# Kernel optimization log

Measured on AMD Instinct MI355X. Metric: run time of the kernel, lower is better.

## Reference

```python
import jax, jax.numpy as jnp
import numpy as np

# Static config (matches init_kwargs / spatial layout)
SHAPES = ((64, 64), (32, 32), (16, 16))   # (H, W) per level, bev=256 at /4,/8,/16
B, HEADS, LEVELS, POINTS, C = 2, 8, 3, 4, 256
HD = C // HEADS
NV = sum(h * w for h, w in SHAPES)        # 5376
NQ = NV
TP = HEADS * LEVELS * POINTS              # 96


def setup_inputs() -> dict:
    key = jax.random.key(0)
    ks = jax.random.split(key, 10)
    s = 1.0 / np.sqrt(C)
    inp = {
        'query': jax.random.normal(ks[0], (B, NQ, C), dtype=jnp.float32),
        'reference_points': jax.random.uniform(ks[1], (B, NQ, 2), dtype=jnp.float32),
        'value': jax.random.normal(ks[2], (B, NV, C), dtype=jnp.float32),
        'Wv': jax.random.normal(ks[3], (C, C), dtype=jnp.float32) * s,
        'bv': jnp.zeros((C,), dtype=jnp.float32),
        # offset proj: small scale so sampling stays local-ish (orig init is 0)
        'Woff': jax.random.normal(ks[4], (TP * 2, C), dtype=jnp.float32) * (0.02 * s),
        'boff': jnp.zeros((TP * 2,), dtype=jnp.float32),
        'Wa': jax.random.normal(ks[5], (TP, C), dtype=jnp.float32) * s,
        'ba': jnp.zeros((TP,), dtype=jnp.float32),
        'Wo': jax.random.normal(ks[6], (C, C), dtype=jnp.float32) * s,
        'bo': jnp.zeros((C,), dtype=jnp.float32),
    }
    return inp


def _msda(query, reference_points, value, Wv, bv, Woff, boff, Wa, ba, Wo, bo):
    Bb, nq, _ = query.shape
    # value projection -> per-head values
    v = (value @ Wv.T + bv).reshape(Bb, NV, HEADS, HD)
    # sampling offsets: (B, NQ, HEADS, LEVELS, POINTS, 2)
    off = (query @ Woff.T + boff).reshape(Bb, nq, HEADS, LEVELS, POINTS, 2)
    # attention weights: softmax over LEVELS*POINTS jointly
    a = (query @ Wa.T + ba).reshape(Bb, nq, HEADS, LEVELS * POINTS)
    a = jax.nn.softmax(a, axis=-1).reshape(Bb, nq, HEADS, LEVELS, POINTS)
    # sampling locations in [0,1] (clamp matches torch .clamp(0,1))
    loc = jnp.clip(reference_points[:, :, None, None, None, :] + off, 0.0, 1.0)

    out = jnp.zeros((Bb, HEADS, nq, HD), dtype=query.dtype)
    start = 0
    for lvl, (H, W) in enumerate(SHAPES):
        n = H * W
        # (B, HEADS, H*W, HD) flattened level feature map per head
        vl = jnp.transpose(v[:, start:start + n].reshape(Bb, H, W, HEADS, HD),
                           (0, 3, 1, 2, 4)).reshape(Bb, HEADS, n, HD)
        loc_l = loc[:, :, :, lvl]                     # (B, NQ, HEADS, K, 2)
        # align_corners=False unnormalization: ((g+1)*size - 1)/2 with g=2*loc-1
        x = loc_l[..., 0] * W - 0.5
        y = loc_l[..., 1] * H - 0.5
        x0 = jnp.floor(x)
        y0 = jnp.floor(y)
        wx1 = x - x0
        wy1 = y - y0
        x0i = x0.astype(jnp.int32)
        y0i = y0.astype(jnp.int32)
        acc = jnp.zeros((Bb, HEADS, nq * POINTS, HD), dtype=query.dtype)
        for dy in (0, 1):
            for dx in (0, 1):
                ix = x0i + dx
                iy = y0i + dy
                wgt = (wx1 if dx else 1.0 - wx1) * (wy1 if dy else 1.0 - wy1)
                # zero padding outside the map (padding_mode='zeros')
                valid = (ix >= 0) & (ix < W) & (iy >= 0) & (iy < H)
                idx = jnp.clip(iy, 0, H - 1) * W + jnp.clip(ix, 0, W - 1)
                idx_t = jnp.transpose(idx, (0, 2, 1, 3)).reshape(Bb, HEADS, nq * POINTS)
                g = jnp.take_along_axis(vl, idx_t[..., None], axis=2)  # (B,H,NQ*K,HD)
                w_t = jnp.transpose(wgt * valid.astype(wgt.dtype),
                                    (0, 2, 1, 3)).reshape(Bb, HEADS, nq * POINTS, 1)
                acc = acc + g * w_t
        aw = jnp.transpose(a[:, :, :, lvl], (0, 2, 1, 3)).reshape(Bb, HEADS, nq * POINTS, 1)
        out = out + (acc * aw).reshape(Bb, HEADS, nq, POINTS, HD).sum(axis=3)
        start += n
    out = jnp.transpose(out, (0, 2, 1, 3)).reshape(Bb, nq, C)
    return out @ Wo.T + bo


def reference(query, reference_points, value, Wv, bv, Woff, boff, Wa, ba, Wo, bo):
    return _msda(query, reference_points, value, Wv, bv, Woff, boff, Wa, ba, Wo, bo)
```

## Files before the change

kernel.cpp:

```cpp
#include <hip/hip_runtime.h>
#include <hip/hip_bf16.h>
#include <cmath>

#define BATCH   2
#define NQ      5376
#define NV      5376
#define CDIM    256
#define HEADS   8
#define HD      32
#define LEVELS  3
#define POINTS  4
#define TP      96
#define MROWS   (BATCH*NQ)
#define NOFF    (TP*2)
#define NQA     (NOFF+TP)

typedef __attribute__((ext_vector_type(8))) short bf16x8;
typedef __attribute__((ext_vector_type(4))) float f32x4;
typedef unsigned short u16;
typedef unsigned int   u32;

#define AS1 __attribute__((address_space(1)))
#define AS3 __attribute__((address_space(3)))

__device__ __forceinline__ void g2lds16(const void* g, void* l) {
    __builtin_amdgcn_global_load_lds((const AS1 void*)g, (AS3 void*)l, 16, 0, 0);
}

__device__ __forceinline__ u16 bf_of(float f) {
    union { __hip_bfloat16 h; u16 s; } u;
    u.h = __float2bfloat16(f);
    return u.s;
}
__device__ __forceinline__ float bf_back(u16 s) {
    return __uint_as_float((u32)s << 16);
}

__device__ __forceinline__ ushort4 cvt_hi(float4 v) {
    ushort4 h;
    h.x = bf_of(v.x); h.y = bf_of(v.y); h.z = bf_of(v.z); h.w = bf_of(v.w);
    return h;
}
__device__ __forceinline__ ushort4 cvt_lo(float4 v, ushort4 h) {
    ushort4 l;
    l.x = bf_of(v.x - bf_back(h.x));
    l.y = bf_of(v.y - bf_back(h.y));
    l.z = bf_of(v.z - bf_back(h.z));
    l.w = bf_of(v.w - bf_back(h.w));
    return l;
}

#define GBM 64
#define GBN 64
#define GBK 32


#define VBLOCKS (168 * 4)
__global__ __launch_bounds__(256) void gemm_vqa_kernel(
    const float* __restrict__ value, const float* __restrict__ Wv,
    const float* __restrict__ bv, u16* __restrict__ vOut,
    const float* __restrict__ query, const float* __restrict__ Woff,
    const float* __restrict__ Wa,
    const float* __restrict__ boff, const float* __restrict__ ba,
    u16* __restrict__ offOut, u16* __restrict__ aOut)
{
    __shared__ u16 sAh[GBM * GBK];
    __shared__ u16 sAl[GBM * GBK];
    __shared__ u16 sBh[GBN * GBK];

    const int bid = blockIdx.x;
    const bool vpath = bid < VBLOCKS;
    int m0, n0;
    if (vpath) { m0 = (bid >> 2) * GBM;           n0 = (bid & 3) * GBN; }
    else       { const int b2 = bid - VBLOCKS;
                 m0 = (b2 / 5) * GBM;             n0 = (b2 % 5) * GBN; }

    const int tid  = threadIdx.x;
    const int lane = tid & 63;
    const int wave = tid >> 6;
    const int wr   = wave & 1;
    const int wc   = wave >> 1;
    const int qm   = lane & 15;
    const int quad = lane >> 4;

    const int srow = tid >> 2;
    const int sc   = (tid & 3) * 8;

    const float* Asrc = (vpath ? value : query) + (size_t)(m0 + srow) * CDIM;
    const float* Bsrc;
    if (vpath) {
        Bsrc = Wv + (size_t)(n0 + srow) * CDIM;
    } else {
        const int rg = min(n0 + srow, NQA - 1);
        Bsrc = (rg < NOFF) ? (Woff + (size_t)rg * CDIM)
                           : (Wa + (size_t)(rg - NOFF) * CDIM);
    }

    f32x4 acc[2][2];
    #pragma unroll
    for (int i = 0; i < 2; ++i)
        #pragma unroll
        for (int j = 0; j < 2; ++j)
            acc[i][j] = (f32x4){0.f, 0.f, 0.f, 0.f};

    for (int k0 = 0; k0 < CDIM; k0 += GBK) {
        const float4 a0 = *reinterpret_cast<const float4*>(&Asrc[k0 + sc]);
        const float4 a1 = *reinterpret_cast<const float4*>(&Asrc[k0 + sc + 4]);
        const ushort4 ah0 = cvt_hi(a0), ah1 = cvt_hi(a1);
        *reinterpret_cast<ushort4*>(&sAh[srow * GBK + sc])     = ah0;
        *reinterpret_cast<ushort4*>(&sAh[srow * GBK + sc + 4]) = ah1;
        if (vpath) {
            *reinterpret_cast<ushort4*>(&sAl[srow * GBK + sc])     = cvt_lo(a0, ah0);
            *reinterpret_cast<ushort4*>(&sAl[srow * GBK + sc + 4]) = cvt_lo(a1, ah1);
        }
        const float4 b0 = *reinterpret_cast<const float4*>(&Bsrc[k0 + sc]);
        const float4 b1 = *reinterpret_cast<const float4*>(&Bsrc[k0 + sc + 4]);
        *reinterpret_cast<ushort4*>(&sBh[srow * GBK + sc])     = cvt_hi(b0);
        *reinterpret_cast<ushort4*>(&sBh[srow * GBK + sc + 4]) = cvt_hi(b1);
        __syncthreads();

        bf16x8 fah[2], fal[2], fbh[2];
        #pragma unroll
        for (int x = 0; x < 2; ++x) {
            const int rm = wr * 32 + x * 16 + qm;
            const int rn = wc * 32 + x * 16 + qm;
            fah[x] = *reinterpret_cast<const bf16x8*>(&sAh[rm * GBK + quad * 8]);
            fbh[x] = *reinterpret_cast<const bf16x8*>(&sBh[rn * GBK + quad * 8]);
            if (vpath)
                fal[x] = *reinterpret_cast<const bf16x8*>(&sAl[rm * GBK + quad * 8]);
        }
        #pragma unroll
        for (int mi = 0; mi < 2; ++mi)
            #pragma unroll
            for (int ni = 0; ni < 2; ++ni) {
                acc[mi][ni] = __builtin_amdgcn_mfma_f32_16x16x32_bf16(
                    fah[mi], fbh[ni], acc[mi][ni], 0, 0, 0);
                if (vpath)
                    acc[mi][ni] = __builtin_amdgcn_mfma_f32_16x16x32_bf16(
                        fal[mi], fbh[ni], acc[mi][ni], 0, 0, 0);
            }
        __syncthreads();
    }

    #pragma unroll
    for (int mi = 0; mi < 2; ++mi) {
        #pragma unroll
        for (int ni = 0; ni < 2; ++ni) {
            const int n = n0 + wc * 32 + ni * 16 + qm;
            if (vpath) {
                const float bn = bv[n];
                #pragma unroll
                for (int r = 0; r < 4; ++r) {
                    const int m = m0 + wr * 32 + mi * 16 + quad * 4 + r;
                    const float val = acc[mi][ni][r] + bn;
                    const int b = m / NV, rr = m - b * NV;
                    const int h = n >> 5, c = n & 31;
                    vOut[(((size_t)b * HEADS + h) * NV + rr) * HD + c] = bf_of(val);
                }
            } else {
                if (n >= NQA) continue;
                const float bn = (n < NOFF) ? boff[n] : ba[n - NOFF];
                #pragma unroll
                for (int r = 0; r < 4; ++r) {
                    const int m = m0 + wr * 32 + mi * 16 + quad * 4 + r;
                    const float val = acc[mi][ni][r] + bn;
                    if (n < NOFF)
                        offOut[(size_t)m * NOFF + n] = bf_of(val);
                    else
                        aOut[(size_t)m * TP + (n - NOFF)] = bf_of(val);
                }
            }
        }
    }
}

__global__ __launch_bounds__(256) void gemm_out_kernel(
    const u16* __restrict__ Ah, const u16* __restrict__ Al,
    const float* __restrict__ Wo, const float* __restrict__ bias,
    float* __restrict__ Cout)
{
    __shared__ u16 sAh[GBM * GBK];
    __shared__ u16 sAl[GBM * GBK];
    __shared__ u16 sBh[GBN * GBK];

    const int bid = blockIdx.x;
    const int m0 = (bid >> 2) * GBM;
    const int n0 = (bid & 3) * GBN;

    const int tid  = threadIdx.x;
    const int lane = tid & 63;
    const int wave = tid >> 6;
    const int wr   = wave & 1;
    const int wc   = wave >> 1;
    const int qm   = lane & 15;
    const int quad = lane >> 4;

    const int arow = (wave << 4) + (lane >> 2);
    const int ak   = (lane & 3) * 8;
    const int srow = tid >> 2;
    const int sc   = (tid & 3) * 8;
    const float* Bsrc = Wo + (size_t)(n0 + srow) * CDIM;

    f32x4 acc[2][2];
    #pragma unroll
    for (int i = 0; i < 2; ++i)
        #pragma unroll
        for (int j = 0; j < 2; ++j)
            acc[i][j] = (f32x4){0.f, 0.f, 0.f, 0.f};

    for (int k0 = 0; k0 < CDIM; k0 += GBK) {
        const size_t ga = (size_t)(m0 + arow) * CDIM + k0 + ak;
        g2lds16(Ah + ga, sAh + wave * 512);
        g2lds16(Al + ga, sAl + wave * 512);
        const float4 b0 = *reinterpret_cast<const float4*>(&Bsrc[k0 + sc]);
        const float4 b1 = *reinterpret_cast<const float4*>(&Bsrc[k0 + sc + 4]);
        *reinterpret_cast<ushort4*>(&sBh[srow * GBK + sc])     = cvt_hi(b0);
        *reinterpret_cast<ushort4*>(&sBh[srow * GBK + sc + 4]) = cvt_hi(b1);
        __syncthreads();

        bf16x8 fah[2], fal[2], fbh[2];
        #pragma unroll
        for (int x = 0; x < 2; ++x) {
            const int rm = wr * 32 + x * 16 + qm;
            const int rn = wc * 32 + x * 16 + qm;
            fah[x] = *reinterpret_cast<const bf16x8*>(&sAh[rm * GBK + quad * 8]);
            fal[x] = *reinterpret_cast<const bf16x8*>(&sAl[rm * GBK + quad * 8]);
            fbh[x] = *reinterpret_cast<const bf16x8*>(&sBh[rn * GBK + quad * 8]);
        }
        #pragma unroll
        for (int mi = 0; mi < 2; ++mi)
            #pragma unroll
            for (int ni = 0; ni < 2; ++ni) {
                acc[mi][ni] = __builtin_amdgcn_mfma_f32_16x16x32_bf16(
                    fah[mi], fbh[ni], acc[mi][ni], 0, 0, 0);
                acc[mi][ni] = __builtin_amdgcn_mfma_f32_16x16x32_bf16(
                    fal[mi], fbh[ni], acc[mi][ni], 0, 0, 0);
            }
        __syncthreads();
    }

    #pragma unroll
    for (int mi = 0; mi < 2; ++mi) {
        #pragma unroll
        for (int ni = 0; ni < 2; ++ni) {
            const int n = n0 + wc * 32 + ni * 16 + qm;
            const float bn = bias[n];
            #pragma unroll
            for (int r = 0; r < 4; ++r) {
                const int m = m0 + wr * 32 + mi * 16 + quad * 4 + r;
                Cout[(size_t)m * CDIM + n] = acc[mi][ni][r] + bn;
            }
        }
    }
}

__global__ __launch_bounds__(256) void msda_core_kernel(
    const u16* __restrict__ off,
    const u16* __restrict__ alog,
    const float* __restrict__ refp,
    const u16*   __restrict__ v,
    u16* __restrict__ t_hi,
    u16* __restrict__ t_lo)
{
    const int tid  = threadIdx.x;
    const int half = tid >> 7;
    const int ht   = tid & 127;
    const int bq   = blockIdx.x * 2 + half;
    const int b    = bq / NQ;

    __shared__ float s_w[2][TP];
    __shared__ int   s_idx[2][TP][4];
    __shared__ float s_twt[2][TP][4];

    if (ht < TP) s_w[half][ht] = bf_back(alog[(size_t)bq * TP + ht]);
    __syncthreads();

    if (ht < HEADS) {
        float mx = -1e30f;
        #pragma unroll
        for (int i = 0; i < 12; ++i) mx = fmaxf(mx, s_w[half][ht * 12 + i]);
        float e[12];
        float sum = 0.f;
        #pragma unroll
        for (int i = 0; i < 12; ++i) {
            e[i] = expf(s_w[half][ht * 12 + i] - mx);
            sum += e[i];
        }
        const float inv = 1.f / sum;
        #pragma unroll
        for (int i = 0; i < 12; ++i) s_w[half][ht * 12 + i] = e[i] * inv;
    }
    __syncthreads();

    if (ht < TP) {
        const int j  = ht;
        const int jj = j % 12;
        const int l  = jj >> 2;
        const int Wl    = (l == 0) ? 64 : (l == 1) ? 32 : 16;
        const int start = (l == 0) ? 0 : (l == 1) ? 4096 : 5120;

        const float refx = refp[(size_t)bq * 2 + 0];
        const float refy = refp[(size_t)bq * 2 + 1];
        const float ox = bf_back(off[(size_t)bq * NOFF + j * 2 + 0]);
        const float oy = bf_back(off[(size_t)bq * NOFF + j * 2 + 1]);
        const float lx = fminf(fmaxf(refx + ox, 0.f), 1.f) * (float)Wl - 0.5f;
        const float ly = fminf(fmaxf(refy + oy, 0.f), 1.f) * (float)Wl - 0.5f;
        const float fx0 = floorf(lx), fy0 = floorf(ly);
        const int   x0  = (int)fx0,   y0  = (int)fy0;
        const float wx1 = lx - fx0,   wy1 = ly - fy0;
        const float wx0 = 1.f - wx1,  wy0 = 1.f - wy1;
        const float aw  = s_w[half][j];

        #pragma unroll
        for (int k = 0; k < 4; ++k) {
            const int dx = k & 1, dy = k >> 1;
            const int xi = x0 + dx, yi = y0 + dy;
            const bool ok = (xi >= 0) & (xi < Wl) & (yi >= 0) & (yi < Wl);
            const int xc = min(max(xi, 0), Wl - 1);
            const int yc = min(max(yi, 0), Wl - 1);
            s_idx[half][j][k] = (start + yc * Wl + xc) * (HD * 2);
            const float wxy = (dx ? wx1 : wx0) * (dy ? wy1 : wy0);
            s_twt[half][j][k] = ok ? aw * wxy : 0.f;
        }
    }
    __syncthreads();

    const int h   = ht >> 4;
    const int sub = ht & 15;
    const int q   = sub & 7;
    const int rep = sub >> 3;
    const char* vb = (const char*)v + (((size_t)b * HEADS + h) * NV) * (HD * 2) + q * 8;

    float acc0 = 0.f, acc1 = 0.f, acc2 = 0.f, acc3 = 0.f;
    #pragma unroll
    for (int g = 0; g < 3; ++g) {
        uint2 raw[8];
        float wt[8];
        #pragma unroll
        for (int pp = 0; pp < 2; ++pp) {
            const int j = h * 12 + rep * 6 + g * 2 + pp;
            const int4   ix = *reinterpret_cast<const int4*>(&s_idx[half][j][0]);
            const float4 tw = *reinterpret_cast<const float4*>(&s_twt[half][j][0]);
            raw[pp * 4 + 0] = *reinterpret_cast<const uint2*>(vb + ix.x);
            raw[pp * 4 + 1] = *reinterpret_cast<const uint2*>(vb + ix.y);
            raw[pp * 4 + 2] = *reinterpret_cast<const uint2*>(vb + ix.z);
            raw[pp * 4 + 3] = *reinterpret_cast<const uint2*>(vb + ix.w);
            wt[pp * 4 + 0] = tw.x; wt[pp * 4 + 1] = tw.y;
            wt[pp * 4 + 2] = tw.z; wt[pp * 4 + 3] = tw.w;
        }
        #pragma unroll
        for (int k = 0; k < 8; ++k) {
            acc0 += wt[k] * __uint_as_float(raw[k].x << 16);
            acc1 += wt[k] * __uint_as_float(raw[k].x & 0xffff0000u);
            acc2 += wt[k] * __uint_as_float(raw[k].y << 16);
            acc3 += wt[k] * __uint_as_float(raw[k].y & 0xffff0000u);
        }
    }

    acc0 += __shfl_xor(acc0, 8);
    acc1 += __shfl_xor(acc1, 8);
    acc2 += __shfl_xor(acc2, 8);
    acc3 += __shfl_xor(acc3, 8);

    if (rep == 0) {
        ushort4 hh, ll;
        hh.x = bf_of(acc0); ll.x = bf_of(acc0 - bf_back(hh.x));
        hh.y = bf_of(acc1); ll.y = bf_of(acc1 - bf_back(hh.y));
        hh.z = bf_of(acc2); ll.z = bf_of(acc2 - bf_back(hh.z));
        hh.w = bf_of(acc3); ll.w = bf_of(acc3 - bf_back(hh.w));
        const size_t base = (size_t)bq * CDIM + h * HD + q * 4;
        *reinterpret_cast<ushort4*>(t_hi + base) = hh;
        *reinterpret_cast<ushort4*>(t_lo + base) = ll;
    }
}

extern "C" void kernel_launch(void* const* d_in, const int* in_sizes, int n_in,
                              void* d_out, int out_size, void* d_ws, size_t ws_size,
                              hipStream_t stream)
{
    const float* query = (const float*)d_in[0];
    const float* refp  = (const float*)d_in[1];
    const float* value = (const float*)d_in[2];
    const float* Wv    = (const float*)d_in[3];
    const float* bv    = (const float*)d_in[4];
    const float* Woff  = (const float*)d_in[5];
    const float* boff  = (const float*)d_in[6];
    const float* Wa    = (const float*)d_in[7];
    const float* ba    = (const float*)d_in[8];
    const float* Wo    = (const float*)d_in[9];
    const float* bo    = (const float*)d_in[10];
    float* out = (float*)d_out;

    char* w = (char*)d_ws;
    const size_t SZ_T = (size_t)MROWS * CDIM * 2;
    u16* v_bf16 = (u16*)(w);
    u16* t_hi   = (u16*)(w + 1 * SZ_T);
    u16* t_lo   = (u16*)(w + 2 * SZ_T);
    u16* ws_off = (u16*)(w + 3 * SZ_T);
    u16* ws_a   = (u16*)(w + 3 * SZ_T + (size_t)MROWS * NOFF * 2);

    const dim3 blk(256);

    gemm_vqa_kernel<<<dim3(VBLOCKS + (MROWS / GBM) * 5), blk, 0, stream>>>(
        value, Wv, bv, v_bf16,
        query, Woff, Wa, boff, ba, ws_off, ws_a);

    msda_core_kernel<<<dim3(MROWS / 2), blk, 0, stream>>>(
        ws_off, ws_a, refp, v_bf16, t_hi, t_lo);

    gemm_out_kernel<<<dim3((MROWS / GBM) * 4), blk, 0, stream>>>(
        t_hi, t_lo, Wo, bo, out);
}
```

Before: 138.9 us.

## Drop lo-part split for sampled output and widen gather to 16-byte loads

The low-residual bf16 tensor for the sampled attention output is removed, so the output GEMM does one MFMA per tile instead of two and reads half the activation data. The sampling kernel now handles four queries per block with 64 threads each, and each lane gathers 8 channels with 16-byte loads instead of 4 with 8-byte loads. This cuts memory traffic and instruction count in both the sampling and the output projection, at the cost of lower precision in the output GEMM inputs.

Result: faster. 135.6 us (-2.4%).

```diff
diff --git a/kernel.cpp b/kernel.cpp
--- a/kernel.cpp
+++ b/kernel.cpp
@@ -53,7 +53,6 @@
 #define GBM 64
 #define GBN 64
 #define GBK 32
-
 
 #define VBLOCKS (168 * 4)
 __global__ __launch_bounds__(256) void gemm_vqa_kernel(
@@ -175,12 +174,11 @@
 }
 
 __global__ __launch_bounds__(256) void gemm_out_kernel(
-    const u16* __restrict__ Ah, const u16* __restrict__ Al,
+    const u16* __restrict__ Ah,
     const float* __restrict__ Wo, const float* __restrict__ bias,
     float* __restrict__ Cout)
 {
     __shared__ u16 sAh[GBM * GBK];
-    __shared__ u16 sAl[GBM * GBK];
     __shared__ u16 sBh[GBN * GBK];
 
     const int bid = blockIdx.x;
@@ -211,31 +209,26 @@
     for (int k0 = 0; k0 < CDIM; k0 += GBK) {
         const size_t ga = (size_t)(m0 + arow) * CDIM + k0 + ak;
         g2lds16(Ah + ga, sAh + wave * 512);
-        g2lds16(Al + ga, sAl + wave * 512);
         const float4 b0 = *reinterpret_cast<const float4*>(&Bsrc[k0 + sc]);
         const float4 b1 = *reinterpret_cast<const float4*>(&Bsrc[k0 + sc + 4]);
         *reinterpret_cast<ushort4*>(&sBh[srow * GBK + sc])     = cvt_hi(b0);
         *reinterpret_cast<ushort4*>(&sBh[srow * GBK + sc + 4]) = cvt_hi(b1);
         __syncthreads();
 
-        bf16x8 fah[2], fal[2], fbh[2];
+        bf16x8 fah[2], fbh[2];
         #pragma unroll
         for (int x = 0; x < 2; ++x) {
             const int rm = wr * 32 + x * 16 + qm;
             const int rn = wc * 32 + x * 16 + qm;
             fah[x] = *reinterpret_cast<const bf16x8*>(&sAh[rm * GBK + quad * 8]);
-            fal[x] = *reinterpret_cast<const bf16x8*>(&sAl[rm * GBK + quad * 8]);
             fbh[x] = *reinterpret_cast<const bf16x8*>(&sBh[rn * GBK + quad * 8]);
         }
         #pragma unroll
         for (int mi = 0; mi < 2; ++mi)
             #pragma unroll
-            for (int ni = 0; ni < 2; ++ni) {
+            for (int ni = 0; ni < 2; ++ni)
                 acc[mi][ni] = __builtin_amdgcn_mfma_f32_16x16x32_bf16(
                     fah[mi], fbh[ni], acc[mi][ni], 0, 0, 0);
-                acc[mi][ni] = __builtin_amdgcn_mfma_f32_16x16x32_bf16(
-                    fal[mi], fbh[ni], acc[mi][ni], 0, 0, 0);
-            }
         __syncthreads();
     }
 
@@ -259,118 +252,133 @@
     const u16* __restrict__ alog,
     const float* __restrict__ refp,
     const u16*   __restrict__ v,
-    u16* __restrict__ t_hi,
-    u16* __restrict__ t_lo)
+    u16* __restrict__ t_hi)
 {
-    const int tid  = threadIdx.x;
-    const int half = tid >> 7;
-    const int ht   = tid & 127;
-    const int bq   = blockIdx.x * 2 + half;
-    const int b    = bq / NQ;
-
-    __shared__ float s_w[2][TP];
-    __shared__ int   s_idx[2][TP][4];
-    __shared__ float s_twt[2][TP][4];
-
-    if (ht < TP) s_w[half][ht] = bf_back(alog[(size_t)bq * TP + ht]);
+    const int tid = threadIdx.x;
+    const int bq0 = blockIdx.x * 4;
+
+    __shared__ float s_w[4][TP];
+    __shared__ int   s_idx[4][TP][4];
+    __shared__ float s_twt[4][TP][4];
+
+    #pragma unroll
+    for (int base = 0; base < 4 * TP; base += 256) {
+        const int idx = base + tid;
+        if (idx < 4 * TP) {
+            const int q = idx / TP, j = idx - q * TP;
+            s_w[q][j] = bf_back(alog[(size_t)(bq0 + q) * TP + j]);
+        }
+    }
     __syncthreads();
 
-    if (ht < HEADS) {
+    if (tid < 32) {
+        const int q = tid >> 3, h = tid & 7;
         float mx = -1e30f;
         #pragma unroll
-        for (int i = 0; i < 12; ++i) mx = fmaxf(mx, s_w[half][ht * 12 + i]);
+        for (int i = 0; i < 12; ++i) mx = fmaxf(mx, s_w[q][h * 12 + i]);
         float e[12];
         float sum = 0.f;
         #pragma unroll
         for (int i = 0; i < 12; ++i) {
-            e[i] = expf(s_w[half][ht * 12 + i] - mx);
+            e[i] = expf(s_w[q][h * 12 + i] - mx);
             sum += e[i];
         }
         const float inv = 1.f / sum;
         #pragma unroll
-        for (int i = 0; i < 12; ++i) s_w[half][ht * 12 + i] = e[i] * inv;
+        for (int i = 0; i < 12; ++i) s_w[q][h * 12 + i] = e[i] * inv;
     }
     __syncthreads();
 
-    if (ht < TP) {
-        const int j  = ht;
-        const int jj = j % 12;
-        const int l  = jj >> 2;
-        const int Wl    = (l == 0) ? 64 : (l == 1) ? 32 : 16;
-        const int start = (l == 0) ? 0 : (l == 1) ? 4096 : 5120;
-
-        const float refx = refp[(size_t)bq * 2 + 0];
-        const float refy = refp[(size_t)bq * 2 + 1];
-        const float ox = bf_back(off[(size_t)bq * NOFF + j * 2 + 0]);
-        const float oy = bf_back(off[(size_t)bq * NOFF + j * 2 + 1]);
-        const float lx = fminf(fmaxf(refx + ox, 0.f), 1.f) * (float)Wl - 0.5f;
-        const float ly = fminf(fmaxf(refy + oy, 0.f), 1.f) * (float)Wl - 0.5f;
-        const float fx0 = floorf(lx), fy0 = floorf(ly);
-        const int   x0  = (int)fx0,   y0  = (int)fy0;
-        const float wx1 = lx - fx0,   wy1 = ly - fy0;
-        const float wx0 = 1.f - wx1,  wy0 = 1.f - wy1;
-        const float aw  = s_w[half][j];
-
-        #pragma unroll
-        for (int k = 0; k < 4; ++k) {
-            const int dx = k & 1, dy = k >> 1;
-            const int xi = x0 + dx, yi = y0 + dy;
-            const bool ok = (xi >= 0) & (xi < Wl) & (yi >= 0) & (yi < Wl);
-            const int xc = min(max(xi, 0), Wl - 1);
-            const int yc = min(max(yi, 0), Wl - 1);
-            s_idx[half][j][k] = (start + yc * Wl + xc) * (HD * 2);
-            const float wxy = (dx ? wx1 : wx0) * (dy ? wy1 : wy0);
-            s_twt[half][j][k] = ok ? aw * wxy : 0.f;
+    #pragma unroll
+    for (int base = 0; base < 4 * TP; base += 256) {
+        const int idx = base + tid;
+        if (idx < 4 * TP) {
+            const int q = idx / TP, j = idx - q * TP;
+            const int bq = bq0 + q;
+            const int jj = j % 12;
+            const int l  = jj >> 2;
+            const int Wl    = (l == 0) ? 64 : (l == 1) ? 32 : 16;
+            const int start = (l == 0) ? 0 : (l == 1) ? 4096 : 5120;
+
+            const float refx = refp[(size_t)bq * 2 + 0];
+            const float refy = refp[(size_t)bq * 2 + 1];
+            const float ox = bf_back(off[(size_t)bq * NOFF + j * 2 + 0]);
+            const float oy = bf_back(off[(size_t)bq * NOFF + j * 2 + 1]);
+            const float lx = fminf(fmaxf(refx + ox, 0.f), 1.f) * (float)Wl - 0.5f;
+            const float ly = fminf(fmaxf(refy + oy, 0.f), 1.f) * (float)Wl - 0.5f;
+            const float fx0 = floorf(lx), fy0 = floorf(ly);
+            const int   x0  = (int)fx0,   y0  = (int)fy0;
+            const float wx1 = lx - fx0,   wy1 = ly - fy0;
+            const float wx0 = 1.f - wx1,  wy0 = 1.f - wy1;
+            const float aw  = s_w[q][j];
+
+            #pragma unroll
+            for (int k = 0; k < 4; ++k) {
+                const int dx = k & 1, dy = k >> 1;
+                const int xi = x0 + dx, yi = y0 + dy;
+                const bool ok = (xi >= 0) & (xi < Wl) & (yi >= 0) & (yi < Wl);
+                const int xc = min(max(xi, 0), Wl - 1);
+                const int yc = min(max(yi, 0), Wl - 1);
+                s_idx[q][j][k] = (start + yc * Wl + xc) * (HD * 2);
+                const float wxy = (dx ? wx1 : wx0) * (dy ? wy1 : wy0);
+                s_twt[q][j][k] = ok ? aw * wxy : 0.f;
+            }
         }
     }
     __syncthreads();
 
-    const int h   = ht >> 4;
-    const int sub = ht & 15;
-    const int q   = sub & 7;
-    const int rep = sub >> 3;
-    const char* vb = (const char*)v + (((size_t)b * HEADS + h) * NV) * (HD * 2) + q * 8;
-
-    float acc0 = 0.f, acc1 = 0.f, acc2 = 0.f, acc3 = 0.f;
+    const int qsel = tid >> 6;
+    const int ht   = tid & 63;
+    const int h    = ht >> 3;
+    const int sub  = ht & 7;
+    const int oct  = sub & 3;
+    const int rep  = sub >> 2;
+    const int bq   = bq0 + qsel;
+    const int b    = bq / NQ;
+    const char* vb = (const char*)v + (((size_t)b * HEADS + h) * NV) * (HD * 2) + oct * 16;
+
+    float acc[8] = {};
     #pragma unroll
     for (int g = 0; g < 3; ++g) {
-        uint2 raw[8];
+        uint4 raw[8];
         float wt[8];
         #pragma unroll
         for (int pp = 0; pp < 2; ++pp) {
             const int j = h * 12 + rep * 6 + g * 2 + pp;
-            const int4   ix = *reinterpret_cast<const int4*>(&s_idx[half][j][0]);
-            const float4 tw = *reinterpret_cast<const float4*>(&s_twt[half][j][0]);
-            raw[pp * 4 + 0] = *reinterpret_cast<const uint2*>(vb + ix.x);
-            raw[pp * 4 + 1] = *reinterpret_cast<const uint2*>(vb + ix.y);
-            raw[pp * 4 + 2] = *reinterpret_cast<const uint2*>(vb + ix.z);
-            raw[pp * 4 + 3] = *reinterpret_cast<const uint2*>(vb + ix.w);
+            const int4   ix = *reinterpret_cast<const int4*>(&s_idx[qsel][j][0]);
+            const float4 tw = *reinterpret_cast<const float4*>(&s_twt[qsel][j][0]);
+            raw[pp * 4 + 0] = *reinterpret_cast<const uint4*>(vb + ix.x);
+            raw[pp * 4 + 1] = *reinterpret_cast<const uint4*>(vb + ix.y);
+            raw[pp * 4 + 2] = *reinterpret_cast<const uint4*>(vb + ix.z);
+            raw[pp * 4 + 3] = *reinterpret_cast<const uint4*>(vb + ix.w);
             wt[pp * 4 + 0] = tw.x; wt[pp * 4 + 1] = tw.y;
             wt[pp * 4 + 2] = tw.z; wt[pp * 4 + 3] = tw.w;
         }
         #pragma unroll
         for (int k = 0; k < 8; ++k) {
-            acc0 += wt[k] * __uint_as_float(raw[k].x << 16);
-            acc1 += wt[k] * __uint_as_float(raw[k].x & 0xffff0000u);
-            acc2 += wt[k] * __uint_as_float(raw[k].y << 16);
-            acc3 += wt[k] * __uint_as_float(raw[k].y & 0xffff0000u);
-        }
-    }
-
-    acc0 += __shfl_xor(acc0, 8);
-    acc1 += __shfl_xor(acc1, 8);
-    acc2 += __shfl_xor(acc2, 8);
-    acc3 += __shfl_xor(acc3, 8);
+            acc[0] += wt[k] * __uint_as_float(raw[k].x << 16);
+            acc[1] += wt[k] * __uint_as_float(raw[k].x & 0xffff0000u);
+            acc[2] += wt[k] * __uint_as_float(raw[k].y << 16);
+            acc[3] += wt[k] * __uint_as_float(raw[k].y & 0xffff0000u);
+            acc[4] += wt[k] * __uint_as_float(raw[k].z << 16);
+            acc[5] += wt[k] * __uint_as_float(raw[k].z & 0xffff0000u);
+            acc[6] += wt[k] * __uint_as_float(raw[k].w << 16);
+            acc[7] += wt[k] * __uint_as_float(raw[k].w & 0xffff0000u);
+        }
+    }
+
+    #pragma unroll
+    for (int c = 0; c < 8; ++c)
+        acc[c] += __shfl_xor(acc[c], 4);
 
     if (rep == 0) {
-        ushort4 hh, ll;
-        hh.x = bf_of(acc0); ll.x = bf_of(acc0 - bf_back(hh.x));
-        hh.y = bf_of(acc1); ll.y = bf_of(acc1 - bf_back(hh.y));
-        hh.z = bf_of(acc2); ll.z = bf_of(acc2 - bf_back(hh.z));
-        hh.w = bf_of(acc3); ll.w = bf_of(acc3 - bf_back(hh.w));
-        const size_t base = (size_t)bq * CDIM + h * HD + q * 4;
-        *reinterpret_cast<ushort4*>(t_hi + base) = hh;
-        *reinterpret_cast<ushort4*>(t_lo + base) = ll;
+        uint4 o;
+        o.x = (u32)bf_of(acc[0]) | ((u32)bf_of(acc[1]) << 16);
+        o.y = (u32)bf_of(acc[2]) | ((u32)bf_of(acc[3]) << 16);
+        o.z = (u32)bf_of(acc[4]) | ((u32)bf_of(acc[5]) << 16);
+        o.w = (u32)bf_of(acc[6]) | ((u32)bf_of(acc[7]) << 16);
+        const size_t base = (size_t)bq * CDIM + h * HD + oct * 8;
+        *reinterpret_cast<uint4*>(t_hi + base) = o;
     }
 }
 
@@ -395,9 +403,8 @@
     const size_t SZ_T = (size_t)MROWS * CDIM * 2;
     u16* v_bf16 = (u16*)(w);
     u16* t_hi   = (u16*)(w + 1 * SZ_T);
-    u16* t_lo   = (u16*)(w + 2 * SZ_T);
-    u16* ws_off = (u16*)(w + 3 * SZ_T);
-    u16* ws_a   = (u16*)(w + 3 * SZ_T + (size_t)MROWS * NOFF * 2);
+    u16* ws_off = (u16*)(w + 2 * SZ_T);
+    u16* ws_a   = (u16*)(w + 2 * SZ_T + (size_t)MROWS * NOFF * 2);
 
     const dim3 blk(256);
 
@@ -405,9 +412,9 @@
         value, Wv, bv, v_bf16,
         query, Woff, Wa, boff, ba, ws_off, ws_a);
 
-    msda_core_kernel<<<dim3(MROWS / 2), blk, 0, stream>>>(
-        ws_off, ws_a, refp, v_bf16, t_hi, t_lo);
+    msda_core_kernel<<<dim3(MROWS / 4), blk, 0, stream>>>(
+        ws_off, ws_a, refp, v_bf16, t_hi);
 
     gemm_out_kernel<<<dim3((MROWS / GBM) * 4), blk, 0, stream>>>(
-        t_hi, t_lo, Wo, bo, out);
-}
+        t_hi, Wo, bo, out);
+}
```
